# Performance work log

Measured on AMD Instinct MI355X. Metric: run time of the kernel, lower is better.

Reference implementation:

```python
import jax, jax.numpy as jnp
import numpy as np

THRESHOLD = 0.1
EPS = 1e-05


def setup_inputs() -> dict:
    key = jax.random.key(0)
    kx, kl, k1, k2 = jax.random.split(key, 4)
    B, S, D = 8, 4096, 1024
    Dh = max(2, D // 2)
    x = jax.random.normal(kx, (B, S, D), dtype=jnp.float32)
    # trailing (right) padding with random valid lengths in [S//2, S]
    lengths = jax.random.randint(kl, (B,), S // 2, S + 1)
    pad = jnp.arange(S)[None, :] >= lengths[:, None]  # [B, S] bool, True = padded
    W1 = jax.random.normal(k1, (D, Dh), dtype=jnp.float32) * (1.0 / np.sqrt(D))
    b1 = jnp.zeros((Dh,), dtype=jnp.float32)
    W2 = jax.random.normal(k2, (Dh, 1), dtype=jnp.float32) * (1.0 / np.sqrt(Dh))
    b2 = jnp.zeros((1,), dtype=jnp.float32)
    return {"x": x, "pad": pad, "W1": W1, "b1": b1, "W2": W2, "b2": b2}


def reference(x, pad, W1, b1, W2, b2):
    B, S, D = x.shape
    pos = jnp.arange(S)
    # number of valid (non-pad) tokens per batch; pad is trailing
    length = S - jnp.sum(pad, axis=1)  # [B]

    # tiny gate MLP: Linear -> ReLU -> Linear, squashed to (0, 1)
    h = jax.nn.relu(jnp.einsum('bsd,dh->bsh', x, W1) + b1)
    y = jnp.einsum('bsh,ho->bso', h, W2) + b2          # [B, S, 1]
    y = (1.0 + jnp.tanh(10.0 * y)) * 0.5

    # zero out gate values at padded positions (torch loop: y[i, n:] = 0)
    valid = pos[None, :] < length[:, None]             # [B, S]
    y = jnp.where(valid[..., None], y, 0.0)

    # lift so at least one token passes the threshold
    adjust = jnp.clip(EPS + THRESHOLD - jnp.max(y, axis=1), 0.0)  # [B, 1]
    y = y + adjust[:, None, :]                         # broadcast over seq

    u = x * y                                          # gated features [B, S, D]
    ys = y[..., 0]                                     # [B, S]
    u_mask = (ys > THRESHOLD) & (~pad)                 # tokens kept
    new_len = jnp.sum(u_mask, axis=1)                  # [B]

    # compact kept tokens to the front of each row (stable sort: kept first,
    # original order preserved) -- the mask-scatter v[v_mask] = u[u_mask]
    order = jnp.argsort(~u_mask, axis=1, stable=True)  # [B, S]
    v = jnp.take_along_axis(u, order[..., None], axis=1)
    v_mask = pos[None, :] < new_len[:, None]           # [B, S]
    v = jnp.where(v_mask[..., None], v, 0.0)
    v_pad = ~v_mask
    return v, v_pad
```

## Files before the change

kernel.cpp:

```cpp
#include <hip/hip_runtime.h>
#include <math.h>

#define NB 8
#define NS 4096
#define ND 1024
#define NDH 512
#define NTOK (NB*NS)
#define THRESH 0.1f
#define EPSV 1e-5f

using short8   = __attribute__((ext_vector_type(8)))  short;
using floatx16 = __attribute__((ext_vector_type(16))) float;
using floatv4  = __attribute__((ext_vector_type(4)))  float;

__device__ __forceinline__ unsigned short f32_to_bf16_rne(float f) {
  union { float f; unsigned u; } v; v.f = f;
  unsigned r = v.u + 0x7fffu + ((v.u >> 16) & 1u);
  return (unsigned short)(r >> 16);
}
__device__ __forceinline__ float bf16_to_f32(unsigned short h) {
  union { unsigned u; float f; } v; v.u = ((unsigned)h) << 16;
  return v.f;
}

__global__ __launch_bounds__(256)
void k0_prep(const float* __restrict__ W1, unsigned short* __restrict__ Wf,
             unsigned int* __restrict__ rowmax) {
  __shared__ float sw[16][513];
  const int t = threadIdx.x;
  const int k16 = blockIdx.x;
  if (k16 == 0 && t < NB) rowmax[t] = 0u;
#pragma unroll
  for (int i = 0; i < 8; ++i) {
    int flat = i * 256 + t;
    int r = flat >> 7, c4 = (flat & 127) << 2;
    *(float4*)&sw[r][c4] = *(const float4*)(W1 + (size_t)(k16 * 16 + r) * NDH + c4);
  }
  __syncthreads();
#pragma unroll
  for (int q = 0; q < 4; ++q) {
    int ss = q * 256 + t;
    int n32 = ss >> 6, lane = ss & 63;
    int n = n32 * 32 + (lane & 31);
    int kb = (lane >> 5) * 8;
    unsigned hi2[4], lo2[4];
#pragma unroll
    for (int j = 0; j < 4; ++j) {
      float w0 = sw[kb + 2 * j][n], w1 = sw[kb + 2 * j + 1][n];
      unsigned short h0 = f32_to_bf16_rne(w0), h1 = f32_to_bf16_rne(w1);
      unsigned short l0 = f32_to_bf16_rne(w0 - bf16_to_f32(h0));
      unsigned short l1 = f32_to_bf16_rne(w1 - bf16_to_f32(h1));
      hi2[j] = (unsigned)h0 | ((unsigned)h1 << 16);
      lo2[j] = (unsigned)l0 | ((unsigned)l1 << 16);
    }
    size_t cb = ((size_t)(n32 * 64 + k16) * 2) * 512 + (size_t)lane * 8;
    *(uint4*)(Wf + cb)       = make_uint4(hi2[0], hi2[1], hi2[2], hi2[3]);
    *(uint4*)(Wf + cb + 512) = make_uint4(lo2[0], lo2[1], lo2[2], lo2[3]);
  }
}

__global__ __launch_bounds__(256, 2)
void k1_gemm(const float* __restrict__ x, const unsigned short* __restrict__ Wf,
             const float* __restrict__ b1, const float* __restrict__ W2,
             const int* __restrict__ pad, const float* __restrict__ b2,
             float* __restrict__ ysq, unsigned int* __restrict__ rowmax) {
  __shared__ __align__(16) unsigned short sx[2][2][64 * 40];
  __shared__ float red[4][64];

  const int tid = threadIdx.x;
  const int wave = tid >> 6, lane = tid & 63;
  const int l31 = lane & 31, h5 = lane >> 5;
  const int tok0 = blockIdx.x * 64;

  floatx16 acc[2][4];
#pragma unroll
  for (int mt = 0; mt < 2; ++mt)
#pragma unroll
    for (int nt = 0; nt < 4; ++nt)
#pragma unroll
      for (int r = 0; r < 16; ++r) acc[mt][nt][r] = 0.f;

  const int sm = tid >> 2;
  const int sk = (tid & 3) * 8;
  const float* xrow = x + (size_t)(tok0 + sm) * ND + sk;

  const unsigned short* wb[4];
#pragma unroll
  for (int nt = 0; nt < 4; ++nt)
    wb[nt] = Wf + (((size_t)(wave * 4 + nt) * 64) * 2) * 512 + (size_t)lane * 8;

  {
    float4 xa = *(const float4*)xrow;
    float4 xb = *(const float4*)(xrow + 4);
    float v8[8] = {xa.x, xa.y, xa.z, xa.w, xb.x, xb.y, xb.z, xb.w};
    unsigned hp[4], lp[4];
#pragma unroll
    for (int j = 0; j < 4; ++j) {
      unsigned short h0 = f32_to_bf16_rne(v8[2 * j]);
      unsigned short h1 = f32_to_bf16_rne(v8[2 * j + 1]);
      unsigned short l0 = f32_to_bf16_rne(v8[2 * j] - bf16_to_f32(h0));
      unsigned short l1 = f32_to_bf16_rne(v8[2 * j + 1] - bf16_to_f32(h1));
      hp[j] = (unsigned)h0 | ((unsigned)h1 << 16);
      lp[j] = (unsigned)l0 | ((unsigned)l1 << 16);
    }
    *(uint4*)&sx[0][0][sm * 40 + sk] = make_uint4(hp[0], hp[1], hp[2], hp[3]);
    *(uint4*)&sx[0][1][sm * 40 + sk] = make_uint4(lp[0], lp[1], lp[2], lp[3]);
  }

  for (int it = 0; it < 32; ++it) {
    const int p = it & 1;
    __syncthreads();
    short8 bh[4][2], bl[4][2];
#pragma unroll
    for (int nt = 0; nt < 4; ++nt)
#pragma unroll
      for (int kh = 0; kh < 2; ++kh) {
        const unsigned short* q = wb[nt] + ((size_t)(2 * it + kh) * 2) * 512;
        bh[nt][kh] = *(const short8*)(q);
        bl[nt][kh] = *(const short8*)(q + 512);
      }
    float4 pxa, pxb;
    if (it < 31) {
      const float* xp = xrow + (it + 1) * 32;
      pxa = *(const float4*)xp;
      pxb = *(const float4*)(xp + 4);
    }
    short8 ah[2][2], al[2][2];
#pragma unroll
    for (int mt = 0; mt < 2; ++mt)
#pragma unroll
      for (int kh = 0; kh < 2; ++kh) {
        ah[mt][kh] = *(const short8*)&sx[p][0][(mt * 32 + l31) * 40 + kh * 16 + h5 * 8];
        al[mt][kh] = *(const short8*)&sx[p][1][(mt * 32 + l31) * 40 + kh * 16 + h5 * 8];
      }
#pragma unroll
    for (int kh = 0; kh < 2; ++kh) {
#pragma unroll
      for (int nt = 0; nt < 4; ++nt)
#pragma unroll
        for (int mt = 0; mt < 2; ++mt)
          acc[mt][nt] = __builtin_amdgcn_mfma_f32_32x32x16_bf16(ah[mt][kh], bh[nt][kh], acc[mt][nt], 0, 0, 0);
#pragma unroll
      for (int nt = 0; nt < 4; ++nt)
#pragma unroll
        for (int mt = 0; mt < 2; ++mt)
          acc[mt][nt] = __builtin_amdgcn_mfma_f32_32x32x16_bf16(al[mt][kh], bh[nt][kh], acc[mt][nt], 0, 0, 0);
#pragma unroll
      for (int nt = 0; nt < 4; ++nt)
#pragma unroll
        for (int mt = 0; mt < 2; ++mt)
          acc[mt][nt] = __builtin_amdgcn_mfma_f32_32x32x16_bf16(ah[mt][kh], bl[nt][kh], acc[mt][nt], 0, 0, 0);
    }
    if (it < 31) {
      float v8[8] = {pxa.x, pxa.y, pxa.z, pxa.w, pxb.x, pxb.y, pxb.z, pxb.w};
      unsigned hp[4], lp[4];
#pragma unroll
      for (int j = 0; j < 4; ++j) {
        unsigned short h0 = f32_to_bf16_rne(v8[2 * j]);
        unsigned short h1 = f32_to_bf16_rne(v8[2 * j + 1]);
        unsigned short l0 = f32_to_bf16_rne(v8[2 * j] - bf16_to_f32(h0));
        unsigned short l1 = f32_to_bf16_rne(v8[2 * j + 1] - bf16_to_f32(h1));
        hp[j] = (unsigned)h0 | ((unsigned)h1 << 16);
        lp[j] = (unsigned)l0 | ((unsigned)l1 << 16);
      }
      *(uint4*)&sx[p ^ 1][0][sm * 40 + sk] = make_uint4(hp[0], hp[1], hp[2], hp[3]);
      *(uint4*)&sx[p ^ 1][1][sm * 40 + sk] = make_uint4(lp[0], lp[1], lp[2], lp[3]);
    }
  }

  float b1v[4], w2v[4];
#pragma unroll
  for (int nt = 0; nt < 4; ++nt) {
    const int n = wave * 128 + nt * 32 + l31;
    b1v[nt] = b1[n];
    w2v[nt] = W2[n];
  }
#pragma unroll
  for (int mt = 0; mt < 2; ++mt) {
    float pr[16];
#pragma unroll
    for (int r = 0; r < 16; ++r) pr[r] = 0.f;
#pragma unroll
    for (int nt = 0; nt < 4; ++nt)
#pragma unroll
      for (int r = 0; r < 16; ++r)
        pr[r] += fmaxf(acc[mt][nt][r] + b1v[nt], 0.f) * w2v[nt];
#pragma unroll
    for (int m = 1; m <= 16; m <<= 1)
#pragma unroll
      for (int r = 0; r < 16; ++r) pr[r] += __shfl_xor(pr[r], m, 64);
    if (l31 == 0) {
#pragma unroll
      for (int r = 0; r < 16; ++r) {
        int row = (r & 3) + 8 * (r >> 2) + 4 * h5;
        red[wave][mt * 32 + row] = pr[r];
      }
    }
  }
  __syncthreads();
  if (tid < 64) {
    float s = red[0][tid] + red[1][tid] + red[2][tid] + red[3][tid];
    const int t = tok0 + tid;
    float yl = s + b2[0];
    float y = (1.f + tanhf(10.f * yl)) * 0.5f;
    if (pad[t]) y = 0.f;
    ysq[t] = y;
    float m = y;
#pragma unroll
    for (int o = 32; o >= 1; o >>= 1) m = fmaxf(m, __shfl_xor(m, o, 64));
    if (tid == 0) atomicMax(rowmax + (t >> 12), __float_as_uint(m));
  }
}

__global__ __launch_bounds__(256)
void k2b(const float* __restrict__ ysq, const int* __restrict__ pad,
         const unsigned int* __restrict__ rowmax, float* __restrict__ gval,
         int* __restrict__ src_of_dest, int* __restrict__ new_len,
         float* __restrict__ vpad_out) {
  __shared__ int ssum[4];
  const int b = blockIdx.x, tid = threadIdx.x;
  const int lane = tid & 63, wv = tid >> 6;
  const int base = b * NS, s0 = tid * 16;
  const float adj = fmaxf(EPSV + THRESH - __uint_as_float(rowmax[b]), 0.f);

  float yv[16];
  unsigned km = 0;
  int cnt = 0;
#pragma unroll
  for (int i = 0; i < 16; ++i) {
    int s = s0 + i;
    float yf = ysq[base + s] + adj;
    yv[i] = yf;
    bool keep = (yf > THRESH) && !pad[base + s];
    if (keep) { km |= (1u << i); ++cnt; }
  }
  int inc = cnt;
#pragma unroll
  for (int o = 1; o < 64; o <<= 1) {
    int tmp = __shfl_up(inc, o, 64);
    if (lane >= o) inc += tmp;
  }
  if (lane == 63) ssum[wv] = inc;
  __syncthreads();
  int wpre = 0;
  for (int w = 0; w < wv; ++w) wpre += ssum[w];
  const int total = ssum[0] + ssum[1] + ssum[2] + ssum[3];
  int off = wpre + inc - cnt;
#pragma unroll
  for (int i = 0; i < 16; ++i) {
    int s = s0 + i;
    if ((km >> i) & 1u) {
      src_of_dest[base + off] = s;
      gval[base + off] = yv[i];
      ++off;
    }
    vpad_out[base + s] = (s >= total) ? 1.f : 0.f;
  }
  if (tid == 0) new_len[b] = total;
}

__global__ __launch_bounds__(256)
void k3_gather(const float* __restrict__ x, const float* __restrict__ gval,
               const int* __restrict__ src_of_dest, const int* __restrict__ new_len,
               float* __restrict__ v) {
  const int slot0 = blockIdx.x * 16;
  const int b = slot0 >> 12;
  const int nl = new_len[b];
  const int tid = threadIdx.x;
#pragma unroll
  for (int i = 0; i < 16; ++i) {
    const int slot = slot0 + i;
    const int dest = slot & (NS - 1);
    floatv4* vo = (floatv4*)(v + (size_t)slot * ND);
    floatv4 r;
    if (dest < nl) {
      const int src = src_of_dest[slot];
      const float g = gval[slot];
      floatv4 xv = ((const floatv4*)(x + ((size_t)b * NS + src) * ND))[tid];
      r = xv * g;
    } else {
      r = (floatv4)(0.f);
    }
    __builtin_nontemporal_store(r, vo + tid);
  }
}

extern "C" void kernel_launch(void* const* d_in, const int* in_sizes, int n_in,
                              void* d_out, int out_size, void* d_ws, size_t ws_size,
                              hipStream_t stream) {
  const float* x   = (const float*)d_in[0];
  const int*   pad = (const int*)d_in[1];
  const float* W1  = (const float*)d_in[2];
  const float* b1  = (const float*)d_in[3];
  const float* W2  = (const float*)d_in[4];
  const float* b2  = (const float*)d_in[5];

  float* v    = (float*)d_out;
  float* vpad = v + (size_t)NTOK * ND;

  unsigned short* Wf = (unsigned short*)(v + 24000000);

  float* ysq  = (float*)d_ws;
  float* gval = ysq + NTOK;
  int* src    = (int*)(gval + NTOK);
  int* nlen   = src + NTOK;
  unsigned int* rowmax = (unsigned int*)(nlen + NB);

  k0_prep<<<64, 256, 0, stream>>>(W1, Wf, rowmax);
  k1_gemm<<<NTOK / 64, 256, 0, stream>>>(x, Wf, b1, W2, pad, b2, ysq, rowmax);
  k2b<<<NB, 256, 0, stream>>>(ysq, pad, rowmax, gval, src, nlen, vpad);
  k3_gather<<<NTOK / 16, 256, 0, stream>>>(x, gval, src, nlen, v);
}
```

Measured before the change: 319.2 us.

## Use 512-thread blocks in gate GEMM with fewer N tiles per wave

The gate GEMM block grows from 4 to 8 waves, and each wave now computes 64 hidden columns instead of 128. This halves the accumulator registers per wave, so more waves can be resident to hide memory latency, and each thread now stages 4 x values instead of 8. MFMA sections are also wrapped with s_setprio to favour the matrix-issuing waves. The cost is more waves rereading the same shared x tile per block, a larger cross-wave reduction, and more per-wave B-fragment loads relative to compute.

```diff
diff --git a/kernel.cpp b/kernel.cpp
--- a/kernel.cpp
+++ b/kernel.cpp
@@ -59,71 +59,69 @@
   }
 }
 
-__global__ __launch_bounds__(256, 2)
+__global__ __launch_bounds__(512, 4)
 void k1_gemm(const float* __restrict__ x, const unsigned short* __restrict__ Wf,
              const float* __restrict__ b1, const float* __restrict__ W2,
              const int* __restrict__ pad, const float* __restrict__ b2,
              float* __restrict__ ysq, unsigned int* __restrict__ rowmax) {
   __shared__ __align__(16) unsigned short sx[2][2][64 * 40];
-  __shared__ float red[4][64];
+  __shared__ float red[8][64];
 
   const int tid = threadIdx.x;
   const int wave = tid >> 6, lane = tid & 63;
   const int l31 = lane & 31, h5 = lane >> 5;
   const int tok0 = blockIdx.x * 64;
 
-  floatx16 acc[2][4];
+  floatx16 acc[2][2];
 #pragma unroll
   for (int mt = 0; mt < 2; ++mt)
 #pragma unroll
-    for (int nt = 0; nt < 4; ++nt)
+    for (int nt = 0; nt < 2; ++nt)
 #pragma unroll
       for (int r = 0; r < 16; ++r) acc[mt][nt][r] = 0.f;
 
-  const int sm = tid >> 2;
-  const int sk = (tid & 3) * 8;
+  const int sm = tid >> 3;
+  const int sk = (tid & 7) * 4;
   const float* xrow = x + (size_t)(tok0 + sm) * ND + sk;
 
-  const unsigned short* wb[4];
-#pragma unroll
-  for (int nt = 0; nt < 4; ++nt)
-    wb[nt] = Wf + (((size_t)(wave * 4 + nt) * 64) * 2) * 512 + (size_t)lane * 8;
+  const unsigned short* wb[2];
+#pragma unroll
+  for (int nt = 0; nt < 2; ++nt)
+    wb[nt] = Wf + (((size_t)(wave * 2 + nt) * 64) * 2) * 512 + (size_t)lane * 8;
 
   {
     float4 xa = *(const float4*)xrow;
-    float4 xb = *(const float4*)(xrow + 4);
-    float v8[8] = {xa.x, xa.y, xa.z, xa.w, xb.x, xb.y, xb.z, xb.w};
-    unsigned hp[4], lp[4];
-#pragma unroll
-    for (int j = 0; j < 4; ++j) {
-      unsigned short h0 = f32_to_bf16_rne(v8[2 * j]);
-      unsigned short h1 = f32_to_bf16_rne(v8[2 * j + 1]);
-      unsigned short l0 = f32_to_bf16_rne(v8[2 * j] - bf16_to_f32(h0));
-      unsigned short l1 = f32_to_bf16_rne(v8[2 * j + 1] - bf16_to_f32(h1));
+    float v4[4] = {xa.x, xa.y, xa.z, xa.w};
+    unsigned hp[2], lp[2];
+#pragma unroll
+    for (int j = 0; j < 2; ++j) {
+      unsigned short h0 = f32_to_bf16_rne(v4[2 * j]);
+      unsigned short h1 = f32_to_bf16_rne(v4[2 * j + 1]);
+      unsigned short l0 = f32_to_bf16_rne(v4[2 * j] - bf16_to_f32(h0));
+      unsigned short l1 = f32_to_bf16_rne(v4[2 * j + 1] - bf16_to_f32(h1));
       hp[j] = (unsigned)h0 | ((unsigned)h1 << 16);
       lp[j] = (unsigned)l0 | ((unsigned)l1 << 16);
     }
-    *(uint4*)&sx[0][0][sm * 40 + sk] = make_uint4(hp[0], hp[1], hp[2], hp[3]);
-    *(uint4*)&sx[0][1][sm * 40 + sk] = make_uint4(lp[0], lp[1], lp[2], lp[3]);
+    *(uint2*)&sx[0][0][sm * 40 + sk] = make_uint2(hp[0], hp[1]);
+    *(uint2*)&sx[0][1][sm * 40 + sk] = make_uint2(lp[0], lp[1]);
   }
 
   for (int it = 0; it < 32; ++it) {
     const int p = it & 1;
     __syncthreads();
-    short8 bh[4][2], bl[4][2];
-#pragma unroll
-    for (int nt = 0; nt < 4; ++nt)
+    short8 bh[2][2], bl[2][2];
+#pragma unroll
+    for (int nt = 0; nt < 2; ++nt)
 #pragma unroll
       for (int kh = 0; kh < 2; ++kh) {
         const unsigned short* q = wb[nt] + ((size_t)(2 * it + kh) * 2) * 512;
         bh[nt][kh] = *(const short8*)(q);
         bl[nt][kh] = *(const short8*)(q + 512);
       }
-    float4 pxa, pxb;
+    float4 pxa;
     if (it < 31) {
       const float* xp = xrow + (it + 1) * 32;
       pxa = *(const float4*)xp;
-      pxb = *(const float4*)(xp + 4);
     }
     short8 ah[2][2], al[2][2];
 #pragma unroll
@@ -133,45 +131,47 @@
         ah[mt][kh] = *(const short8*)&sx[p][0][(mt * 32 + l31) * 40 + kh * 16 + h5 * 8];
         al[mt][kh] = *(const short8*)&sx[p][1][(mt * 32 + l31) * 40 + kh * 16 + h5 * 8];
       }
+    __builtin_amdgcn_s_setprio(1);
 #pragma unroll
     for (int kh = 0; kh < 2; ++kh) {
 #pragma unroll
-      for (int nt = 0; nt < 4; ++nt)
+      for (int nt = 0; nt < 2; ++nt)
 #pragma unroll
         for (int mt = 0; mt < 2; ++mt)
           acc[mt][nt] = __builtin_amdgcn_mfma_f32_32x32x16_bf16(ah[mt][kh], bh[nt][kh], acc[mt][nt], 0, 0, 0);
 #pragma unroll
-      for (int nt = 0; nt < 4; ++nt)
+      for (int nt = 0; nt < 2; ++nt)
 #pragma unroll
         for (int mt = 0; mt < 2; ++mt)
           acc[mt][nt] = __builtin_amdgcn_mfma_f32_32x32x16_bf16(al[mt][kh], bh[nt][kh], acc[mt][nt], 0, 0, 0);
 #pragma unroll
-      for (int nt = 0; nt < 4; ++nt)
+      for (int nt = 0; nt < 2; ++nt)
 #pragma unroll
         for (int mt = 0; mt < 2; ++mt)
           acc[mt][nt] = __builtin_amdgcn_mfma_f32_32x32x16_bf16(ah[mt][kh], bl[nt][kh], acc[mt][nt], 0, 0, 0);
     }
+    __builtin_amdgcn_s_setprio(0);
     if (it < 31) {
-      float v8[8] = {pxa.x, pxa.y, pxa.z, pxa.w, pxb.x, pxb.y, pxb.z, pxb.w};
-      unsigned hp[4], lp[4];
-#pragma unroll
-      for (int j = 0; j < 4; ++j) {
-        unsigned short h0 = f32_to_bf16_rne(v8[2 * j]);
-        unsigned short h1 = f32_to_bf16_rne(v8[2 * j + 1]);
-        unsigned short l0 = f32_to_bf16_rne(v8[2 * j] - bf16_to_f32(h0));
-        unsigned short l1 = f32_to_bf16_rne(v8[2 * j + 1] - bf16_to_f32(h1));
+      float v4[4] = {pxa.x, pxa.y, pxa.z, pxa.w};
+      unsigned hp[2], lp[2];
+#pragma unroll
+      for (int j = 0; j < 2; ++j) {
+        unsigned short h0 = f32_to_bf16_rne(v4[2 * j]);
+        unsigned short h1 = f32_to_bf16_rne(v4[2 * j + 1]);
+        unsigned short l0 = f32_to_bf16_rne(v4[2 * j] - bf16_to_f32(h0));
+        unsigned short l1 = f32_to_bf16_rne(v4[2 * j + 1] - bf16_to_f32(h1));
         hp[j] = (unsigned)h0 | ((unsigned)h1 << 16);
         lp[j] = (unsigned)l0 | ((unsigned)l1 << 16);
       }
-      *(uint4*)&sx[p ^ 1][0][sm * 40 + sk] = make_uint4(hp[0], hp[1], hp[2], hp[3]);
-      *(uint4*)&sx[p ^ 1][1][sm * 40 + sk] = make_uint4(lp[0], lp[1], lp[2], lp[3]);
-    }
-  }
-
-  float b1v[4], w2v[4];
-#pragma unroll
-  for (int nt = 0; nt < 4; ++nt) {
-    const int n = wave * 128 + nt * 32 + l31;
+      *(uint2*)&sx[p ^ 1][0][sm * 40 + sk] = make_uint2(hp[0], hp[1]);
+      *(uint2*)&sx[p ^ 1][1][sm * 40 + sk] = make_uint2(lp[0], lp[1]);
+    }
+  }
+
+  float b1v[2], w2v[2];
+#pragma unroll
+  for (int nt = 0; nt < 2; ++nt) {
+    const int n = wave * 64 + nt * 32 + l31;
     b1v[nt] = b1[n];
     w2v[nt] = W2[n];
   }
@@ -181,7 +181,7 @@
 #pragma unroll
     for (int r = 0; r < 16; ++r) pr[r] = 0.f;
 #pragma unroll
-    for (int nt = 0; nt < 4; ++nt)
+    for (int nt = 0; nt < 2; ++nt)
 #pragma unroll
       for (int r = 0; r < 16; ++r)
         pr[r] += fmaxf(acc[mt][nt][r] + b1v[nt], 0.f) * w2v[nt];
@@ -199,7 +199,8 @@
   }
   __syncthreads();
   if (tid < 64) {
-    float s = red[0][tid] + red[1][tid] + red[2][tid] + red[3][tid];
+    float s = red[0][tid] + red[1][tid] + red[2][tid] + red[3][tid]
+            + red[4][tid] + red[5][tid] + red[6][tid] + red[7][tid];
     const int t = tok0 + tid;
     float yl = s + b2[0];
     float y = (1.f + tanhf(10.f * yl)) * 0.5f;
@@ -307,7 +308,7 @@
   unsigned int* rowmax = (unsigned int*)(nlen + NB);
 
   k0_prep<<<64, 256, 0, stream>>>(W1, Wf, rowmax);
-  k1_gemm<<<NTOK / 64, 256, 0, stream>>>(x, Wf, b1, W2, pad, b2, ysq, rowmax);
+  k1_gemm<<<NTOK / 64, 512, 0, stream>>>(x, Wf, b1, W2, pad, b2, ysq, rowmax);
   k2b<<<NB, 256, 0, stream>>>(ysq, pad, rowmax, gval, src, nlen, vpad);
   k3_gather<<<NTOK / 16, 256, 0, stream>>>(x, gval, src, nlen, v);
 }
```

After: 963.1 us. 3.02x slower.

## Load x fragments directly into registers, dropping LDS staging and barriers

Applied to the files above, without the earlier changes.

The GEMM kernel no longer stages converted x tiles through double-buffered shared memory. Each wave now loads its own A-fragment rows straight from global memory into registers, splits them into bf16 hi/lo, and prefetches the next k-step into a second register set. This removes the per-iteration __syncthreads and LDS traffic. In exchange, all four waves redundantly load and convert the same x data, which raises global/L2 traffic, conversion ALU work and register pressure.

```diff
diff --git a/kernel.cpp b/kernel.cpp
--- a/kernel.cpp
+++ b/kernel.cpp
@@ -23,6 +23,23 @@
   return v.f;
 }
 
+__device__ __forceinline__ void cvt8_split(const float4& a, const float4& b,
+                                           short8& hi, short8& lo) {
+  float v8[8] = {a.x, a.y, a.z, a.w, b.x, b.y, b.z, b.w};
+  unsigned hp[4], lp[4];
+#pragma unroll
+  for (int j = 0; j < 4; ++j) {
+    unsigned short h0 = f32_to_bf16_rne(v8[2 * j]);
+    unsigned short h1 = f32_to_bf16_rne(v8[2 * j + 1]);
+    unsigned short l0 = f32_to_bf16_rne(v8[2 * j] - bf16_to_f32(h0));
+    unsigned short l1 = f32_to_bf16_rne(v8[2 * j + 1] - bf16_to_f32(h1));
+    hp[j] = (unsigned)h0 | ((unsigned)h1 << 16);
+    lp[j] = (unsigned)l0 | ((unsigned)l1 << 16);
+  }
+  *(uint4*)&hi = make_uint4(hp[0], hp[1], hp[2], hp[3]);
+  *(uint4*)&lo = make_uint4(lp[0], lp[1], lp[2], lp[3]);
+}
+
 __global__ __launch_bounds__(256)
 void k0_prep(const float* __restrict__ W1, unsigned short* __restrict__ Wf,
              unsigned int* __restrict__ rowmax) {
@@ -64,7 +81,6 @@
              const float* __restrict__ b1, const float* __restrict__ W2,
              const int* __restrict__ pad, const float* __restrict__ b2,
              float* __restrict__ ysq, unsigned int* __restrict__ rowmax) {
-  __shared__ __align__(16) unsigned short sx[2][2][64 * 40];
   __shared__ float red[4][64];
 
   const int tid = threadIdx.x;
@@ -80,91 +96,71 @@
 #pragma unroll
       for (int r = 0; r < 16; ++r) acc[mt][nt][r] = 0.f;
 
-  const int sm = tid >> 2;
-  const int sk = (tid & 3) * 8;
-  const float* xrow = x + (size_t)(tok0 + sm) * ND + sk;
+  const float* xbase = x + (size_t)(tok0 + l31) * ND + h5 * 8;
 
   const unsigned short* wb[4];
 #pragma unroll
   for (int nt = 0; nt < 4; ++nt)
     wb[nt] = Wf + (((size_t)(wave * 4 + nt) * 64) * 2) * 512 + (size_t)lane * 8;
 
-  {
-    float4 xa = *(const float4*)xrow;
-    float4 xb = *(const float4*)(xrow + 4);
-    float v8[8] = {xa.x, xa.y, xa.z, xa.w, xb.x, xb.y, xb.z, xb.w};
-    unsigned hp[4], lp[4];
-#pragma unroll
-    for (int j = 0; j < 4; ++j) {
-      unsigned short h0 = f32_to_bf16_rne(v8[2 * j]);
-      unsigned short h1 = f32_to_bf16_rne(v8[2 * j + 1]);
-      unsigned short l0 = f32_to_bf16_rne(v8[2 * j] - bf16_to_f32(h0));
-      unsigned short l1 = f32_to_bf16_rne(v8[2 * j + 1] - bf16_to_f32(h1));
-      hp[j] = (unsigned)h0 | ((unsigned)h1 << 16);
-      lp[j] = (unsigned)l0 | ((unsigned)l1 << 16);
-    }
-    *(uint4*)&sx[0][0][sm * 40 + sk] = make_uint4(hp[0], hp[1], hp[2], hp[3]);
-    *(uint4*)&sx[0][1][sm * 40 + sk] = make_uint4(lp[0], lp[1], lp[2], lp[3]);
-  }
+  float4 xc[2][2][2], xn[2][2][2];
+#pragma unroll
+  for (int mt = 0; mt < 2; ++mt)
+#pragma unroll
+    for (int kh = 0; kh < 2; ++kh) {
+      const float* xp = xbase + (size_t)mt * 32 * ND + kh * 16;
+      xc[mt][kh][0] = *(const float4*)xp;
+      xc[mt][kh][1] = *(const float4*)(xp + 4);
+    }
 
   for (int it = 0; it < 32; ++it) {
-    const int p = it & 1;
-    __syncthreads();
-    short8 bh[4][2], bl[4][2];
-#pragma unroll
-    for (int nt = 0; nt < 4; ++nt)
-#pragma unroll
-      for (int kh = 0; kh < 2; ++kh) {
+    if (it < 31) {
+#pragma unroll
+      for (int mt = 0; mt < 2; ++mt)
+#pragma unroll
+        for (int kh = 0; kh < 2; ++kh) {
+          const float* xp = xbase + (size_t)mt * 32 * ND + (it + 1) * 32 + kh * 16;
+          xn[mt][kh][0] = *(const float4*)xp;
+          xn[mt][kh][1] = *(const float4*)(xp + 4);
+        }
+    }
+#pragma unroll
+    for (int kh = 0; kh < 2; ++kh) {
+      short8 bh[4], bl[4];
+#pragma unroll
+      for (int nt = 0; nt < 4; ++nt) {
         const unsigned short* q = wb[nt] + ((size_t)(2 * it + kh) * 2) * 512;
-        bh[nt][kh] = *(const short8*)(q);
-        bl[nt][kh] = *(const short8*)(q + 512);
+        bh[nt] = *(const short8*)(q);
+        bl[nt] = *(const short8*)(q + 512);
       }
-    float4 pxa, pxb;
+      short8 ah[2], al[2];
+#pragma unroll
+      for (int mt = 0; mt < 2; ++mt)
+        cvt8_split(xc[mt][kh][0], xc[mt][kh][1], ah[mt], al[mt]);
+#pragma unroll
+      for (int nt = 0; nt < 4; ++nt)
+#pragma unroll
+        for (int mt = 0; mt < 2; ++mt)
+          acc[mt][nt] = __builtin_amdgcn_mfma_f32_32x32x16_bf16(ah[mt], bh[nt], acc[mt][nt], 0, 0, 0);
+#pragma unroll
+      for (int nt = 0; nt < 4; ++nt)
+#pragma unroll
+        for (int mt = 0; mt < 2; ++mt)
+          acc[mt][nt] = __builtin_amdgcn_mfma_f32_32x32x16_bf16(al[mt], bh[nt], acc[mt][nt], 0, 0, 0);
+#pragma unroll
+      for (int nt = 0; nt < 4; ++nt)
+#pragma unroll
+        for (int mt = 0; mt < 2; ++mt)
+          acc[mt][nt] = __builtin_amdgcn_mfma_f32_32x32x16_bf16(ah[mt], bl[nt], acc[mt][nt], 0, 0, 0);
+    }
     if (it < 31) {
-      const float* xp = xrow + (it + 1) * 32;
-      pxa = *(const float4*)xp;
-      pxb = *(const float4*)(xp + 4);
-    }
-    short8 ah[2][2], al[2][2];
-#pragma unroll
-    for (int mt = 0; mt < 2; ++mt)
-#pragma unroll
-      for (int kh = 0; kh < 2; ++kh) {
-        ah[mt][kh] = *(const short8*)&sx[p][0][(mt * 32 + l31) * 40 + kh * 16 + h5 * 8];
-        al[mt][kh] = *(const short8*)&sx[p][1][(mt * 32 + l31) * 40 + kh * 16 + h5 * 8];
-      }
-#pragma unroll
-    for (int kh = 0; kh < 2; ++kh) {
-#pragma unroll
-      for (int nt = 0; nt < 4; ++nt)
-#pragma unroll
-        for (int mt = 0; mt < 2; ++mt)
-          acc[mt][nt] = __builtin_amdgcn_mfma_f32_32x32x16_bf16(ah[mt][kh], bh[nt][kh], acc[mt][nt], 0, 0, 0);
-#pragma unroll
-      for (int nt = 0; nt < 4; ++nt)
-#pragma unroll
-        for (int mt = 0; mt < 2; ++mt)
-          acc[mt][nt] = __builtin_amdgcn_mfma_f32_32x32x16_bf16(al[mt][kh], bh[nt][kh], acc[mt][nt], 0, 0, 0);
-#pragma unroll
-      for (int nt = 0; nt < 4; ++nt)
-#pragma unroll
-        for (int mt = 0; mt < 2; ++mt)
-          acc[mt][nt] = __builtin_amdgcn_mfma_f32_32x32x16_bf16(ah[mt][kh], bl[nt][kh], acc[mt][nt], 0, 0, 0);
-    }
-    if (it < 31) {
-      float v8[8] = {pxa.x, pxa.y, pxa.z, pxa.w, pxb.x, pxb.y, pxb.z, pxb.w};
-      unsigned hp[4], lp[4];
-#pragma unroll
-      for (int j = 0; j < 4; ++j) {
-        unsigned short h0 = f32_to_bf16_rne(v8[2 * j]);
-        unsigned short h1 = f32_to_bf16_rne(v8[2 * j + 1]);
-        unsigned short l0 = f32_to_bf16_rne(v8[2 * j] - bf16_to_f32(h0));
-        unsigned short l1 = f32_to_bf16_rne(v8[2 * j + 1] - bf16_to_f32(h1));
-        hp[j] = (unsigned)h0 | ((unsigned)h1 << 16);
-        lp[j] = (unsigned)l0 | ((unsigned)l1 << 16);
-      }
-      *(uint4*)&sx[p ^ 1][0][sm * 40 + sk] = make_uint4(hp[0], hp[1], hp[2], hp[3]);
-      *(uint4*)&sx[p ^ 1][1][sm * 40 + sk] = make_uint4(lp[0], lp[1], lp[2], lp[3]);
+#pragma unroll
+      for (int mt = 0; mt < 2; ++mt)
+#pragma unroll
+        for (int kh = 0; kh < 2; ++kh) {
+          xc[mt][kh][0] = xn[mt][kh][0];
+          xc[mt][kh][1] = xn[mt][kh][1];
+        }
     }
   }
 
```

Measured after the change: 335.7 us. +5.2%, slower.
